# Kernel optimization log

Hardware: AMD Instinct MI355X
Metric: run time of the kernel (lower is better)

The kernel has to match this reference:

```python
import jax, jax.numpy as jnp
import numpy as np

IN_FEATURES = 3
CODE_NUM = 64
CODE_CHANNEL = 64
SHAPE_NUM = 1


def setup_inputs() -> dict:
    key = jax.random.key(0)
    k1, k2 = jax.random.split(key)
    coords = jax.random.uniform(k1, (8, 65536, IN_FEATURES), dtype=jnp.float32)  # in [0,1) subset of [-1,1]
    table_size = SHAPE_NUM * CODE_NUM ** IN_FEATURES
    # xavier_uniform for [C, N] matrix
    limit = float(np.sqrt(6.0 / (CODE_CHANNEL + table_size)))
    shape_code = jax.random.uniform(k2, (CODE_CHANNEL, table_size), dtype=jnp.float32,
                                    minval=-limit, maxval=limit)
    return {"coords": coords, "shape_code": shape_code, "idx": 0}


def reference(coords, shape_code, idx):
    D = IN_FEATURES
    # corner offset mask: [2^D, D] of {0,1}
    mask = jnp.stack(jnp.meshgrid(*([jnp.arange(2, dtype=jnp.float32)] * D), indexing="ij"), -1)
    mask = mask.reshape(-1, D)                                   # [8, 3]
    mul = jnp.asarray([CODE_NUM ** i for i in range(D)], dtype=jnp.int64)
    offset = jnp.asarray(idx, dtype=jnp.int64) * (CODE_NUM ** D)

    c = (coords + 1.0) * ((CODE_NUM - 1) / 2.0)                  # [B, P, 3] in [0, code_num-1]
    corners = jnp.floor(c)[..., None, :] + mask                  # [B, P, 8, 3]
    coordsf = c[..., None, :] - corners                          # [B, P, 8, 3]
    index = jnp.sum(corners.astype(jnp.int64) * mul, axis=-1) + offset  # [B, P, 8]
    weights = jnp.prod(1.0 - jnp.abs(coordsf), axis=-1)          # [B, P, 8]

    code = jnp.take(shape_code, index, axis=1)                   # [C, B, P, 8] gather
    out = jnp.einsum("cbpk,bpk->bpc", code, weights)             # weighted corner sum
    return out
```

## Files before the change

kernel.cpp:

```cpp
#include <hip/hip_runtime.h>


#define CODE_NUM 64
#define CODE_CHANNEL 64
#define TABLE (CODE_NUM * CODE_NUM * CODE_NUM)

__global__ __launch_bounds__(256) void transpose_k(const float* __restrict__ src,
                                                   float* __restrict__ dst) {
    __shared__ float tile[64 * 65];
    const int t0 = blockIdx.x * 64;
    const int j = threadIdx.x;

#pragma unroll
    for (int i = 0; i < 4; ++i) {
        const int q = (i << 8) | j;
        const int c = q >> 4;
        const int tc4 = q & 15;
        const float4 v = *(const float4*)(src + (size_t)c * TABLE + t0 + (tc4 << 2));
        tile[((tc4 << 2) + 0) * 65 + c] = v.x;
        tile[((tc4 << 2) + 1) * 65 + c] = v.y;
        tile[((tc4 << 2) + 2) * 65 + c] = v.z;
        tile[((tc4 << 2) + 3) * 65 + c] = v.w;
    }
    __syncthreads();

#pragma unroll
    for (int i = 0; i < 4; ++i) {
        const int q = (i << 8) | j;
        const int t = q >> 4;
        const int c4 = q & 15;
        float4 v;
        v.x = tile[t * 65 + (c4 << 2) + 0];
        v.y = tile[t * 65 + (c4 << 2) + 1];
        v.z = tile[t * 65 + (c4 << 2) + 2];
        v.w = tile[t * 65 + (c4 << 2) + 3];
        *(float4*)(dst + (size_t)(t0 + t) * 64 + (c4 << 2)) = v;
    }
}

__global__ __launch_bounds__(256) void interp4_k(const float* __restrict__ coords,
                                                 const float* __restrict__ table,
                                                 const int* __restrict__ idxp,
                                                 float* __restrict__ out,
                                                 int npoints) {
    const unsigned tid = blockIdx.x * 256u + threadIdx.x;
    const int lane = threadIdx.x & 63;
    const int sub = lane >> 4;
    const int cg = lane & 15;
    const int p = (int)((tid >> 6) * 4u + (unsigned)sub);
    if (p >= npoints) return;

    const int offset = idxp[0] * TABLE;

    const float sx = (coords[p * 3 + 0] + 1.0f) * ((CODE_NUM - 1) * 0.5f);
    const float sy = (coords[p * 3 + 1] + 1.0f) * ((CODE_NUM - 1) * 0.5f);
    const float sz = (coords[p * 3 + 2] + 1.0f) * ((CODE_NUM - 1) * 0.5f);

    const float fx = floorf(sx), fy = floorf(sy), fz = floorf(sz);
    const float rx = sx - fx, ry = sy - fy, rz = sz - fz;
    const int ix = (int)fx, iy = (int)fy, iz = (int)fz;
    const int base = offset + ix + iy * CODE_NUM + iz * (CODE_NUM * CODE_NUM);

    const float wx[2] = {1.0f - rx, rx};
    const float wy[2] = {1.0f - ry, ry};
    const float wz[2] = {1.0f - rz, rz};

    const char* tp = (const char*)table;
    const int cgoff = cg << 4;

    float4 acc = make_float4(0.f, 0.f, 0.f, 0.f);
#pragma unroll
    for (int k = 0; k < 8; ++k) {
        const int a = k & 1, b = (k >> 1) & 1, c = (k >> 2) & 1;
        const int idx = base + a + b * CODE_NUM + c * (CODE_NUM * CODE_NUM);
        const float w = wx[a] * wy[b] * wz[c];
        const float4 v = *(const float4*)(tp + ((size_t)(unsigned)(idx << 8) + cgoff));
        acc.x = fmaf(w, v.x, acc.x);
        acc.y = fmaf(w, v.y, acc.y);
        acc.z = fmaf(w, v.z, acc.z);
        acc.w = fmaf(w, v.w, acc.w);
    }
    *(float4*)(out + (size_t)p * CODE_CHANNEL + (cg << 2)) = acc;
}

__global__ __launch_bounds__(256) void interp_fallback_k(const float* __restrict__ coords,
                                                         const float* __restrict__ table,
                                                         const int* __restrict__ idxp,
                                                         float* __restrict__ out,
                                                         int npoints) {
    const int p = (int)((blockIdx.x * 256u + threadIdx.x) >> 6);
    const int lane = threadIdx.x & 63;
    if (p >= npoints) return;
    const int offset = idxp[0] * TABLE;
    const float sx = (coords[p * 3 + 0] + 1.0f) * ((CODE_NUM - 1) * 0.5f);
    const float sy = (coords[p * 3 + 1] + 1.0f) * ((CODE_NUM - 1) * 0.5f);
    const float sz = (coords[p * 3 + 2] + 1.0f) * ((CODE_NUM - 1) * 0.5f);
    const float fx = floorf(sx), fy = floorf(sy), fz = floorf(sz);
    const float rx = sx - fx, ry = sy - fy, rz = sz - fz;
    const int base = offset + (int)fx + (int)fy * CODE_NUM + (int)fz * (CODE_NUM * CODE_NUM);
    const float wx[2] = {1.0f - rx, rx};
    const float wy[2] = {1.0f - ry, ry};
    const float wz[2] = {1.0f - rz, rz};
    float acc = 0.0f;
#pragma unroll
    for (int k = 0; k < 8; ++k) {
        const int a = k & 1, b = (k >> 1) & 1, c = (k >> 2) & 1;
        const int idx = base + a + b * CODE_NUM + c * (CODE_NUM * CODE_NUM);
        acc = fmaf(wx[a] * wy[b] * wz[c], table[(size_t)lane * TABLE + idx], acc);
    }
    out[(size_t)p * CODE_CHANNEL + lane] = acc;
}

extern "C" void kernel_launch(void* const* d_in, const int* in_sizes, int n_in,
                              void* d_out, int out_size, void* d_ws, size_t ws_size,
                              hipStream_t stream) {
    const float* coords = (const float*)d_in[0];
    const float* code   = (const float*)d_in[1];
    const int*   idxp   = (const int*)d_in[2];
    float* out = (float*)d_out;

    const int npoints = in_sizes[0] / 3;
    const size_t tbytes = (size_t)TABLE * CODE_CHANNEL * sizeof(float);

    if (ws_size >= tbytes) {
        float* tt = (float*)d_ws;
        transpose_k<<<TABLE / 64, 256, 0, stream>>>(code, tt);
        interp4_k<<<(npoints + 15) / 16, 256, 0, stream>>>(coords, tt, idxp, out, npoints);
    } else {
        interp_fallback_k<<<(npoints + 3) / 4, 256, 0, stream>>>(coords, code, idxp, out, npoints);
    }
}
```

Baseline: 280.9 us.

## Counting-sort points by grid cell before gathering for table locality

```diff
diff --git a/kernel.cpp b/kernel.cpp
--- a/kernel.cpp
+++ b/kernel.cpp
@@ -4,13 +4,15 @@
 #define CODE_NUM 64
 #define CODE_CHANNEL 64
 #define TABLE (CODE_NUM * CODE_NUM * CODE_NUM)
+#define NCELLS TABLE
+
+typedef unsigned int uint;
 
 __global__ __launch_bounds__(256) void transpose_k(const float* __restrict__ src,
                                                    float* __restrict__ dst) {
     __shared__ float tile[64 * 65];
     const int t0 = blockIdx.x * 64;
     const int j = threadIdx.x;
-
 #pragma unroll
     for (int i = 0; i < 4; ++i) {
         const int q = (i << 8) | j;
@@ -23,7 +25,6 @@
         tile[((tc4 << 2) + 3) * 65 + c] = v.w;
     }
     __syncthreads();
-
 #pragma unroll
     for (int i = 0; i < 4; ++i) {
         const int q = (i << 8) | j;
@@ -38,6 +39,120 @@
     }
 }
 
+__device__ __forceinline__ int cell_of(const float* coords, int p,
+                                       float& sx, float& sy, float& sz) {
+    sx = (coords[p * 3 + 0] + 1.0f) * ((CODE_NUM - 1) * 0.5f);
+    sy = (coords[p * 3 + 1] + 1.0f) * ((CODE_NUM - 1) * 0.5f);
+    sz = (coords[p * 3 + 2] + 1.0f) * ((CODE_NUM - 1) * 0.5f);
+    const int ix = (int)floorf(sx), iy = (int)floorf(sy), iz = (int)floorf(sz);
+    return ix + iy * CODE_NUM + iz * (CODE_NUM * CODE_NUM);
+}
+
+__global__ __launch_bounds__(256) void hist_k(const float* __restrict__ coords,
+                                              uint* __restrict__ hist, int npoints) {
+    const int p = blockIdx.x * 256 + threadIdx.x;
+    if (p >= npoints) return;
+    float sx, sy, sz;
+    const int cell = cell_of(coords, p, sx, sy, sz);
+    atomicAdd(&hist[cell], 1u);
+}
+
+__global__ __launch_bounds__(256) void scan_a(const uint* __restrict__ hist,
+                                              uint* __restrict__ base,
+                                              uint* __restrict__ aux) {
+    __shared__ uint s[256];
+    const int b = blockIdx.x, t = threadIdx.x;
+    const uint4 h = ((const uint4*)hist)[b * 256 + t];
+    const uint sum = h.x + h.y + h.z + h.w;
+    s[t] = sum;
+    __syncthreads();
+    for (int off = 1; off < 256; off <<= 1) {
+        const uint v = (t >= off) ? s[t - off] : 0u;
+        __syncthreads();
+        s[t] += v;
+        __syncthreads();
+    }
+    const uint incl = s[t];
+    const uint excl = incl - sum;
+    uint4 e;
+    e.x = excl; e.y = excl + h.x; e.z = e.y + h.y; e.w = e.z + h.z;
+    ((uint4*)base)[b * 256 + t] = e;
+    if (t == 255) aux[b] = incl;
+}
+
+__global__ __launch_bounds__(256) void scan_b(uint* __restrict__ aux) {
+    __shared__ uint s[256];
+    const int t = threadIdx.x;
+    const uint v = aux[t];
+    s[t] = v;
+    __syncthreads();
+    for (int off = 1; off < 256; off <<= 1) {
+        const uint u = (t >= off) ? s[t - off] : 0u;
+        __syncthreads();
+        s[t] += u;
+        __syncthreads();
+    }
+    aux[t] = s[t] - v;
+}
+
+__global__ __launch_bounds__(256) void scatter_k(const float* __restrict__ coords,
+                                                 uint* __restrict__ hist,
+                                                 const uint* __restrict__ base,
+                                                 const uint* __restrict__ aux,
+                                                 float4* __restrict__ sorted,
+                                                 int npoints) {
+    const int p = blockIdx.x * 256 + threadIdx.x;
+    if (p >= npoints) return;
+    float sx, sy, sz;
+    const int cell = cell_of(coords, p, sx, sy, sz);
+    const uint start = base[cell] + aux[cell >> 10];
+    const uint r = atomicSub(&hist[cell], 1u) - 1u;
+    sorted[start + r] = make_float4(sx, sy, sz, __int_as_float(p));
+}
+
+__global__ __launch_bounds__(256) void interp_sorted_k(const float4* __restrict__ sorted,
+                                                       const float* __restrict__ table,
+                                                       const int* __restrict__ idxp,
+                                                       float* __restrict__ out,
+                                                       int npoints) {
+    const unsigned tid = blockIdx.x * 256u + threadIdx.x;
+    const int lane = threadIdx.x & 63;
+    const int sub = lane >> 4;
+    const int cg = lane & 15;
+    const int j = (int)((tid >> 6) * 4u + (unsigned)sub);
+    if (j >= npoints) return;
+
+    const float4 f = sorted[j];
+    const float sx = f.x, sy = f.y, sz = f.z;
+    const int p = __float_as_int(f.w);
+
+    const int offset = idxp[0] * TABLE;
+    const float fx = floorf(sx), fy = floorf(sy), fz = floorf(sz);
+    const float rx = sx - fx, ry = sy - fy, rz = sz - fz;
+    const int base = offset + (int)fx + (int)fy * CODE_NUM + (int)fz * (CODE_NUM * CODE_NUM);
+
+    const float wx[2] = {1.0f - rx, rx};
+    const float wy[2] = {1.0f - ry, ry};
+    const float wz[2] = {1.0f - rz, rz};
+
+    const char* tp = (const char*)table;
+    const int cgoff = cg << 4;
+
+    float4 acc = make_float4(0.f, 0.f, 0.f, 0.f);
+#pragma unroll
+    for (int k = 0; k < 8; ++k) {
+        const int a = k & 1, b = (k >> 1) & 1, c = (k >> 2) & 1;
+        const int idx = base + a + b * CODE_NUM + c * (CODE_NUM * CODE_NUM);
+        const float w = wx[a] * wy[b] * wz[c];
+        const float4 v = *(const float4*)(tp + ((size_t)(unsigned)(idx << 8) + cgoff));
+        acc.x = fmaf(w, v.x, acc.x);
+        acc.y = fmaf(w, v.y, acc.y);
+        acc.z = fmaf(w, v.z, acc.z);
+        acc.w = fmaf(w, v.w, acc.w);
+    }
+    *(float4*)(out + (size_t)p * CODE_CHANNEL + (cg << 2)) = acc;
+}
+
 __global__ __launch_bounds__(256) void interp4_k(const float* __restrict__ coords,
                                                  const float* __restrict__ table,
                                                  const int* __restrict__ idxp,
@@ -49,25 +164,16 @@
     const int cg = lane & 15;
     const int p = (int)((tid >> 6) * 4u + (unsigned)sub);
     if (p >= npoints) return;
-
     const int offset = idxp[0] * TABLE;
-
-    const float sx = (coords[p * 3 + 0] + 1.0f) * ((CODE_NUM - 1) * 0.5f);
-    const float sy = (coords[p * 3 + 1] + 1.0f) * ((CODE_NUM - 1) * 0.5f);
-    const float sz = (coords[p * 3 + 2] + 1.0f) * ((CODE_NUM - 1) * 0.5f);
-
-    const float fx = floorf(sx), fy = floorf(sy), fz = floorf(sz);
-    const float rx = sx - fx, ry = sy - fy, rz = sz - fz;
-    const int ix = (int)fx, iy = (int)fy, iz = (int)fz;
-    const int base = offset + ix + iy * CODE_NUM + iz * (CODE_NUM * CODE_NUM);
-
+    float sx, sy, sz;
+    const int cell = cell_of(coords, p, sx, sy, sz);
+    const float rx = sx - floorf(sx), ry = sy - floorf(sy), rz = sz - floorf(sz);
+    const int base = offset + cell;
     const float wx[2] = {1.0f - rx, rx};
     const float wy[2] = {1.0f - ry, ry};
     const float wz[2] = {1.0f - rz, rz};
-
     const char* tp = (const char*)table;
     const int cgoff = cg << 4;
-
     float4 acc = make_float4(0.f, 0.f, 0.f, 0.f);
 #pragma unroll
     for (int k = 0; k < 8; ++k) {
@@ -92,12 +198,10 @@
     const int lane = threadIdx.x & 63;
     if (p >= npoints) return;
     const int offset = idxp[0] * TABLE;
-    const float sx = (coords[p * 3 + 0] + 1.0f) * ((CODE_NUM - 1) * 0.5f);
-    const float sy = (coords[p * 3 + 1] + 1.0f) * ((CODE_NUM - 1) * 0.5f);
-    const float sz = (coords[p * 3 + 2] + 1.0f) * ((CODE_NUM - 1) * 0.5f);
-    const float fx = floorf(sx), fy = floorf(sy), fz = floorf(sz);
-    const float rx = sx - fx, ry = sy - fy, rz = sz - fz;
-    const int base = offset + (int)fx + (int)fy * CODE_NUM + (int)fz * (CODE_NUM * CODE_NUM);
+    float sx, sy, sz;
+    const int cell = cell_of(coords, p, sx, sy, sz);
+    const float rx = sx - floorf(sx), ry = sy - floorf(sy), rz = sz - floorf(sz);
+    const int base = offset + cell;
     const float wx[2] = {1.0f - rx, rx};
     const float wy[2] = {1.0f - ry, ry};
     const float wz[2] = {1.0f - rz, rz};
@@ -120,10 +224,34 @@
     float* out = (float*)d_out;
 
     const int npoints = in_sizes[0] / 3;
+    const size_t MB = 1024ull * 1024ull;
     const size_t tbytes = (size_t)TABLE * CODE_CHANNEL * sizeof(float);
 
-    if (ws_size >= tbytes) {
-        float* tt = (float*)d_ws;
+    const size_t off_sorted = tbytes;
+    const size_t off_hist = off_sorted + (size_t)npoints * 16;
+    const size_t off_base = off_hist + (size_t)NCELLS * 4;
+    const size_t off_aux  = off_base + (size_t)NCELLS * 4;
+    const size_t need = off_aux + 4096;
+
+    char* ws = (char*)d_ws;
+    const int pblocks = (npoints + 255) / 256;
+
+    if (ws_size >= need) {
+        float*  tt     = (float*)(ws);
+        float4* sorted = (float4*)(ws + off_sorted);
+        uint*   hist   = (uint*)(ws + off_hist);
+        uint*   basep  = (uint*)(ws + off_base);
+        uint*   aux    = (uint*)(ws + off_aux);
+
+        hipMemsetAsync(hist, 0, (size_t)NCELLS * 4, stream);
+        transpose_k<<<TABLE / 64, 256, 0, stream>>>(code, tt);
+        hist_k<<<pblocks, 256, 0, stream>>>(coords, hist, npoints);
+        scan_a<<<256, 256, 0, stream>>>(hist, basep, aux);
+        scan_b<<<1, 256, 0, stream>>>(aux);
+        scatter_k<<<pblocks, 256, 0, stream>>>(coords, hist, basep, aux, sorted, npoints);
+        interp_sorted_k<<<(npoints + 15) / 16, 256, 0, stream>>>(sorted, tt, idxp, out, npoints);
+    } else if (ws_size >= tbytes) {
+        float* tt = (float*)ws;
         transpose_k<<<TABLE / 64, 256, 0, stream>>>(code, tt);
         interp4_k<<<(npoints + 15) / 16, 256, 0, stream>>>(coords, tt, idxp, out, npoints);
     } else {
```

Result: slower. 326.7 us (+16.3%).
